# Performance work log

Measured on AMD Instinct MI355X. Metric: run time of the kernel, lower is better.

Reference implementation:

```python
import jax, jax.numpy as jnp
import numpy as np

D_MODEL = 1024
D_INNER = 2048      # expand=2 * d_model
HEADDIM = 64
NHEADS = D_INNER // HEADDIM   # 32 (ssm heads)
D_STATE = 128
D_CONV = 4
CHUNK = 256
D_IN_PROJ = 2 * D_INNER + 2 * D_STATE + NHEADS
CONV_DIM = D_INNER + 2 * D_STATE


def setup_inputs() -> dict:
    key = jax.random.key(0)
    ks = jax.random.split(key, 8)
    sc = lambda f: 1.0 / np.sqrt(f)
    dt_init = jax.random.uniform(ks[3], (NHEADS,), minval=0.001, maxval=0.1)
    return {
        "x": jax.random.normal(ks[0], (2, 4096, D_MODEL), jnp.float32),
        "W_in": jax.random.normal(ks[1], (D_MODEL, D_IN_PROJ), jnp.float32) * sc(D_MODEL),
        "conv_w": jax.random.normal(ks[2], (CONV_DIM, D_CONV), jnp.float32) * sc(D_CONV),
        "conv_b": jnp.zeros((CONV_DIM,), jnp.float32),
        "dt_bias": jnp.log(jnp.expm1(dt_init)),            # inverse softplus
        "A_log": jnp.log(jax.random.uniform(ks[4], (NHEADS,), minval=1.0, maxval=16.0)),
        "D": jnp.ones((NHEADS,), jnp.float32),
        "norm_w": jnp.ones((D_INNER,), jnp.float32),
        "W_out": jax.random.normal(ks[5], (D_INNER, D_MODEL), jnp.float32) * sc(D_INNER),
    }


def _segsum(a):
    # a: (..., T) -> (..., T, T) lower-triangular segment sums, -inf above diag
    T = a.shape[-1]
    cs = jnp.cumsum(a, axis=-1)
    diff = cs[..., :, None] - cs[..., None, :]
    mask = jnp.tril(jnp.ones((T, T), bool))
    return jnp.where(mask, diff, -jnp.inf)


def _ssd(x, A, B, C):
    # x: (b,L,h,p) already scaled by dt; A: (b,L,h) = dt*A_head; B,C: (b,L,n)
    b, L, h, p = x.shape
    nc = L // CHUNK
    xc = x.reshape(b, nc, CHUNK, h, p)
    Ac = A.reshape(b, nc, CHUNK, h).transpose(0, 3, 1, 2)      # (b,h,nc,cl)
    Bc = B.reshape(b, nc, CHUNK, -1)
    Cc = C.reshape(b, nc, CHUNK, -1)
    Acs = jnp.cumsum(Ac, axis=-1)
    # intra-chunk (diagonal) term
    Ldec = jnp.exp(_segsum(Ac))                                # (b,h,nc,cl,cl)
    Yd = jnp.einsum('bcln,bcsn,bhcls,bcshp->bclhp', Cc, Bc, Ldec, xc)
    # chunk end states
    decay_states = jnp.exp(Acs[..., -1:] - Acs)                # (b,h,nc,cl)
    states = jnp.einsum('bcln,bhcl,bclhp->bchpn', Bc, decay_states, xc)
    # inter-chunk recurrence (zero initial state)
    states = jnp.concatenate([jnp.zeros_like(states[:, :1]), states], axis=1)
    A_chunk = jnp.pad(Acs[..., -1], ((0, 0), (0, 0), (1, 0)))  # (b,h,nc+1)
    decay_chunk = jnp.exp(_segsum(A_chunk))                    # (b,h,nc+1,nc+1)
    states = jnp.einsum('bhzc,bchpn->bzhpn', decay_chunk, states)[:, :-1]
    # state -> output term
    out_decay = jnp.exp(Acs)                                   # (b,h,nc,cl)
    Yo = jnp.einsum('bcln,bchpn,bhcl->bclhp', Cc, states, out_decay)
    return (Yd + Yo).reshape(b, L, h, p)


def reference(x, W_in, conv_w, conv_b, dt_bias, A_log, D, norm_w, W_out):
    b, L, _ = x.shape
    zxbcdt = x @ W_in                                          # (b,L,4384)
    z, xBC, dt = jnp.split(zxbcdt, [D_INNER, 2 * D_INNER + 2 * D_STATE], axis=-1)
    # causal depthwise conv1d + silu
    xp = jnp.pad(xBC, ((0, 0), (D_CONV - 1, 0), (0, 0)))
    conv = sum(xp[:, k:k + L] * conv_w[:, k] for k in range(D_CONV)) + conv_b
    xBC = jax.nn.silu(conv)
    xs, B, C = jnp.split(xBC, [D_INNER, D_INNER + D_STATE], axis=-1)
    dt = jax.nn.softplus(dt + dt_bias)                         # (b,L,h)
    A = -jnp.exp(A_log)                                        # (h,)
    xh = xs.reshape(b, L, NHEADS, HEADDIM)
    y = _ssd(xh * dt[..., None], dt * A, B, C)                 # (b,L,h,p)
    y = y + xh * D[None, None, :, None]                        # D skip per head
    y = y.reshape(b, L, D_INNER)
    # gated RMSNorm
    u = y * jax.nn.silu(z)
    u = u * jax.lax.rsqrt(jnp.mean(u * u, axis=-1, keepdims=True) + 1e-5) * norm_w
    return u @ W_out
```

## Files before the change

kernel.cpp:

```cpp
#include <hip/hip_runtime.h>
#include <math.h>

#define B_ 2
#define L_ 4096
#define DM 1024
#define DI 2048
#define HD 64
#define NH 32
#define DS 128
#define CH 256
#define NC 16
#define DPROJ 4384
#define CONVD 2304
#define NGEMM 4352

typedef unsigned short u16;
typedef unsigned int u32;
typedef __attribute__((ext_vector_type(8))) short bf16x8;
typedef __attribute__((ext_vector_type(4))) float f32x4;

__device__ __forceinline__ float silu_(float x) { return x / (1.0f + __expf(-x)); }
__device__ __forceinline__ float us2f(u16 u) {
  union { u32 i; float f; } c; c.i = ((u32)u) << 16; return c.f;
}
__device__ __forceinline__ u16 f2us(float f) {
  union { float f; u32 i; } c; c.f = f;
  u32 i = c.i;
  return (u16)((i + 0x7FFFu + ((i >> 16) & 1u)) >> 16);
}
__device__ __forceinline__ void unpack8(uint4 v, float* o) {
  o[0] = us2f(v.x & 0xffffu); o[1] = us2f(v.x >> 16);
  o[2] = us2f(v.y & 0xffffu); o[3] = us2f(v.y >> 16);
  o[4] = us2f(v.z & 0xffffu); o[5] = us2f(v.z >> 16);
  o[6] = us2f(v.w & 0xffffu); o[7] = us2f(v.w >> 16);
}
__device__ __forceinline__ bf16x8 scale8(bf16x8 a, float s) {
  bf16x8 r;
#pragma unroll
  for (int j = 0; j < 8; ++j) r[j] = (short)f2us(us2f((u16)a[j]) * s);
  return r;
}
__device__ __forceinline__ void gload16(const u16* g, u16* l) {
  __builtin_amdgcn_global_load_lds(
      (const __attribute__((address_space(1))) void*)g,
      (__attribute__((address_space(3))) void*)l, 16, 0, 0);
}

__global__ __launch_bounds__(256) void cvt_t_k(const float* __restrict__ W,
                                               u16* __restrict__ Wt,
                                               int ldW, int ldT) {
  __shared__ float tile[64][65];
  const int t = threadIdx.x;
  const int n0 = blockIdx.x * 64, k0 = blockIdx.y * 64;
#pragma unroll
  for (int i = 0; i < 16; ++i) {
    int j = i * 256 + t;
    int kk = j >> 6, nn = j & 63;
    tile[kk][nn] = W[(size_t)(k0 + kk) * ldW + n0 + nn];
  }
  __syncthreads();
#pragma unroll
  for (int i = 0; i < 16; ++i) {
    int j = i * 256 + t;
    int nn = j >> 6, kk = j & 63;
    Wt[(size_t)(n0 + nn) * ldT + k0 + kk] = f2us(tile[kk][nn]);
  }
}

template <int KDIM, int NTN, int EPI>
__global__ __launch_bounds__(256) void gemm_bf16_k(const u16* __restrict__ A,
                                                   const u16* __restrict__ Bt,
                                                   u16* __restrict__ zb,
                                                   u16* __restrict__ xraw,
                                                   float* __restrict__ outf,
                                                   int nwg) {
  __shared__ u16 pool[(EPI == 1) ? 17408 : 16384];
  u16* Al = pool;
  u16* Bl = pool + 8192;
  const int t = threadIdx.x;
  const int wv = t >> 6, lane = t & 63;
  const int fr = lane & 15, oct = lane >> 4;
  const int wr = wv >> 1, wc = wv & 1;
  const int q = nwg >> 3;
  const int wg = (blockIdx.x & 7) * q + (blockIdx.x >> 3);
  const int bm = wg / NTN, bn = wg % NTN;
  const int m0 = bm * 128, n0 = bn * 128;

  const int lr = lane >> 3, ls = lane & 7;
  const int gslot = (ls ^ lr) * 8;

  f32x4 acc[4][4];
#pragma unroll
  for (int mm = 0; mm < 4; ++mm)
#pragma unroll
    for (int nn = 0; nn < 4; ++nn) acc[mm][nn] = (f32x4){0.f, 0.f, 0.f, 0.f};

  for (int k0 = 0; k0 < KDIM; k0 += 64) {
    if (k0) __syncthreads();
#pragma unroll
    for (int i = 0; i < 4; ++i) {
      const int rowA = wv * 32 + i * 8;
      gload16(&A[(size_t)(m0 + rowA + lr) * KDIM + k0 + gslot], &Al[rowA * 64]);
      gload16(&Bt[(size_t)(n0 + rowA + lr) * KDIM + k0 + gslot], &Bl[rowA * 64]);
    }
    __syncthreads();
#pragma unroll
    for (int kk = 0; kk < 2; ++kk) {
      bf16x8 af[4], bfr[4];
#pragma unroll
      for (int mm = 0; mm < 4; ++mm)
        af[mm] = *(const bf16x8*)&Al[(wr * 64 + mm * 16 + fr) * 64 +
                                     (((kk * 4 + oct) ^ (fr & 7)) * 8)];
#pragma unroll
      for (int nn = 0; nn < 4; ++nn)
        bfr[nn] = *(const bf16x8*)&Bl[(wc * 64 + nn * 16 + fr) * 64 +
                                      (((kk * 4 + oct) ^ (fr & 7)) * 8)];
#pragma unroll
      for (int mm = 0; mm < 4; ++mm)
#pragma unroll
        for (int nn = 0; nn < 4; ++nn)
          acc[mm][nn] = __builtin_amdgcn_mfma_f32_16x16x32_bf16(af[mm], bfr[nn],
                                                                acc[mm][nn], 0, 0, 0);
    }
  }

  if (EPI == 0) {
    const bool isz = (n0 < DI);
#pragma unroll
    for (int P = 0; P < 2; ++P) {
      __syncthreads();
      u16* Oh = pool;
      if (wr == P) {
#pragma unroll
        for (int mm = 0; mm < 4; ++mm)
#pragma unroll
          for (int i = 0; i < 4; ++i) {
            int rloc = mm * 16 + oct * 4 + i;
#pragma unroll
            for (int nn = 0; nn < 4; ++nn)
              Oh[rloc * 136 + wc * 64 + nn * 16 + fr] = f2us(acc[mm][nn][i]);
          }
      }
      __syncthreads();
#pragma unroll
      for (int p = 0; p < 4; ++p) {
        int e = p * 256 + t;
        int row = e >> 4, cs = (e & 15) * 8;
        uint4 v = *(const uint4*)&Oh[row * 136 + cs];
        size_t grow = m0 + P * 64 + row;
        int col = n0 + cs;
        if (isz) *(uint4*)&zb[grow * DI + col] = v;
        else     *(uint4*)&xraw[grow * CONVD + (col - DI)] = v;
      }
    }
  } else {
#pragma unroll
    for (int P = 0; P < 2; ++P) {
      __syncthreads();
      float* Of = (float*)pool;
      if (wr == P) {
#pragma unroll
        for (int mm = 0; mm < 4; ++mm)
#pragma unroll
          for (int i = 0; i < 4; ++i) {
            int rloc = mm * 16 + oct * 4 + i;
#pragma unroll
            for (int nn = 0; nn < 4; ++nn)
              Of[rloc * 132 + wc * 64 + nn * 16 + fr] = acc[mm][nn][i];
          }
      }
      __syncthreads();
#pragma unroll
      for (int p = 0; p < 8; ++p) {
        int e = p * 256 + t;
        int row = e >> 5, c4 = (e & 31) * 4;
        float4 v = *(const float4*)&Of[row * 132 + c4];
        *(float4*)&outf[(size_t)(m0 + P * 64 + row) * DM + n0 + c4] = v;
      }
    }
  }
}

__global__ __launch_bounds__(256) void dt_gemm_k(const float* __restrict__ x,
                                                 const float* __restrict__ W,
                                                 const float* __restrict__ dtb,
                                                 float* __restrict__ dtp,
                                                 u16* __restrict__ xb16) {
  __shared__ float xs[8 * 1024];
  const int t = threadIdx.x;
  const int row0 = blockIdx.x * 8;
#pragma unroll
  for (int i = 0; i < 8; ++i) {
    int j4 = i * 256 + t;
    float4 v = *(const float4*)&x[(size_t)row0 * DM + j4 * 4];
    *(float4*)&xs[j4 * 4] = v;
    u32 lo = (u32)f2us(v.x) | ((u32)f2us(v.y) << 16);
    u32 hi = (u32)f2us(v.z) | ((u32)f2us(v.w) << 16);
    *(uint2*)&xb16[(size_t)row0 * DM + j4 * 4] = make_uint2(lo, hi);
  }
  __syncthreads();
  const int r = t >> 5, h = t & 31;
  float a0 = 0.f, a1 = 0.f, a2 = 0.f, a3 = 0.f;
  const float* wcol = W + (DI + CONVD) + h;
  const float* xr = &xs[r * 1024];
  for (int k = 0; k < 1024; k += 4) {
    float4 xv = *(const float4*)&xr[k];
    a0 += xv.x * wcol[(size_t)(k + 0) * DPROJ];
    a1 += xv.y * wcol[(size_t)(k + 1) * DPROJ];
    a2 += xv.z * wcol[(size_t)(k + 2) * DPROJ];
    a3 += xv.w * wcol[(size_t)(k + 3) * DPROJ];
  }
  float v = (a0 + a1) + (a2 + a3) + dtb[h];
  dtp[(size_t)(row0 + r) * NH + h] = (v > 20.0f) ? v : log1pf(__expf(v));
}

__global__ __launch_bounds__(256) void conv_silu_k(const u16* __restrict__ xraw,
                                                   const float* __restrict__ cw,
                                                   const float* __restrict__ cb,
                                                   u16* __restrict__ xbc) {
  int idx = blockIdx.x * 256 + threadIdx.x;
  int ch8 = idx % (CONVD / 8);
  int bl = idx / (CONVD / 8);
  int l = bl & (L_ - 1);
  int ch = ch8 * 8;
  const u16* src = xraw + (size_t)bl * CONVD + ch;
  float a[8], o[8];
#pragma unroll
  for (int qq = 0; qq < 8; ++qq) a[qq] = cb[ch + qq];
  float w0[8], w1[8], w2[8], w3[8];
#pragma unroll
  for (int qq = 0; qq < 8; ++qq) {
    float4 w = *(const float4*)&cw[(ch + qq) * 4];
    w0[qq] = w.x; w1[qq] = w.y; w2[qq] = w.z; w3[qq] = w.w;
  }
  if (l >= 3) {
    uint4 v = *(const uint4*)&src[-3 * CONVD]; unpack8(v, o);
#pragma unroll
    for (int qq = 0; qq < 8; ++qq) a[qq] += o[qq] * w0[qq];
  }
  if (l >= 2) {
    uint4 v = *(const uint4*)&src[-2 * CONVD]; unpack8(v, o);
#pragma unroll
    for (int qq = 0; qq < 8; ++qq) a[qq] += o[qq] * w1[qq];
  }
  if (l >= 1) {
    uint4 v = *(const uint4*)&src[-CONVD]; unpack8(v, o);
#pragma unroll
    for (int qq = 0; qq < 8; ++qq) a[qq] += o[qq] * w2[qq];
  }
  {
    uint4 v = *(const uint4*)&src[0]; unpack8(v, o);
#pragma unroll
    for (int qq = 0; qq < 8; ++qq) a[qq] += o[qq] * w3[qq];
  }
  uint4 ov;
  ov.x = (u32)f2us(silu_(a[0])) | ((u32)f2us(silu_(a[1])) << 16);
  ov.y = (u32)f2us(silu_(a[2])) | ((u32)f2us(silu_(a[3])) << 16);
  ov.z = (u32)f2us(silu_(a[4])) | ((u32)f2us(silu_(a[5])) << 16);
  ov.w = (u32)f2us(silu_(a[6])) | ((u32)f2us(silu_(a[7])) << 16);
  *(uint4*)&xbc[(size_t)bl * CONVD + ch] = ov;
}

__global__ __launch_bounds__(256) void acs_k(const float* __restrict__ dtp,
                                             const float* __restrict__ A_log,
                                             float* __restrict__ Acs) {
  const int t = threadIdx.x;
  const int lane = t & 63, wv = t >> 6;
  const int idx = blockIdx.x * 4 + wv;
  const int h = (idx >> 4) & (NH - 1);
  const int c = idx & (NC - 1);
  const int b = idx >> 9;
  const float Ah = -__expf(A_log[h]);
  const size_t base = ((size_t)b * L_ + c * CH + lane * 4) * NH + h;
  float v0 = dtp[base] * Ah;
  float v1 = dtp[base + NH] * Ah;
  float v2 = dtp[base + 2 * NH] * Ah;
  float v3 = dtp[base + 3 * NH] * Ah;
  float c1 = v0 + v1, c2 = c1 + v2, c3 = c2 + v3;
  float tot = c3;
#pragma unroll
  for (int off = 1; off < 64; off <<= 1) {
    float p = __shfl_up(tot, off, 64);
    if (lane >= off) tot += p;
  }
  float excl = tot - c3;
  float4 ov = make_float4(excl + v0, excl + c1, excl + c2, excl + c3);
  *(float4*)&Acs[(size_t)idx * CH + lane * 4] = ov;
}

#define SLP 72
__global__ __launch_bounds__(256) void states_k(const u16* __restrict__ xbc,
                                                const float* __restrict__ dtp,
                                                const float* __restrict__ Acs,
                                                u16* __restrict__ st16) {
  __shared__ u16 BtT[128 * SLP];
  __shared__ u16 XtT[64 * SLP];
  const int t = threadIdx.x;
  const int wv = t >> 6, lane = t & 63;
  const int fr = lane & 15, oct = lane >> 4;
  const int h = blockIdx.x & 31, c = (blockIdx.x >> 5) & 15, b = blockIdx.x >> 9;
  const size_t acsb = (((size_t)b * NH + h) * NC + c) * CH;
  const float acs_last = Acs[acsb + (CH - 1)];
  const size_t rowbase = (size_t)b * L_ + c * CH;

  f32x4 acc[2][4];
#pragma unroll
  for (int mt = 0; mt < 2; ++mt)
#pragma unroll
    for (int pt = 0; pt < 4; ++pt) acc[mt][pt] = (f32x4){0.f, 0.f, 0.f, 0.f};

  for (int lt = 0; lt < 4; ++lt) {
    __syncthreads();
#pragma unroll
    for (int i = 0; i < 4; ++i) {
      int ci = i * 256 + t;
      int l = ci >> 4, nk = ci & 15;
      uint4 v = *(const uint4*)&xbc[(rowbase + lt * 64 + l) * CONVD + DI + nk * 8];
      u16 p8[8];
      p8[0] = (u16)(v.x & 0xffffu); p8[1] = (u16)(v.x >> 16);
      p8[2] = (u16)(v.y & 0xffffu); p8[3] = (u16)(v.y >> 16);
      p8[4] = (u16)(v.z & 0xffffu); p8[5] = (u16)(v.z >> 16);
      p8[6] = (u16)(v.w & 0xffffu); p8[7] = (u16)(v.w >> 16);
#pragma unroll
      for (int qq = 0; qq < 8; ++qq) {
        int r = nk * 8 + qq;
        BtT[r * SLP + ((((l >> 3) ^ (r >> 3)) & 7) << 3) + (l & 7)] = p8[qq];
      }
    }
#pragma unroll
    for (int i = 0; i < 2; ++i) {
      int ci = i * 256 + t;
      int l = ci >> 3, pk = ci & 7;
      size_t row = rowbase + lt * 64 + l;
      uint4 v = *(const uint4*)&xbc[row * CONVD + h * HD + pk * 8];
      float d = dtp[row * NH + h] * __expf(acs_last - Acs[acsb + lt * 64 + l]);
      float o[8]; unpack8(v, o);
#pragma unroll
      for (int qq = 0; qq < 8; ++qq) {
        int r = pk * 8 + qq;
        XtT[r * SLP + ((((l >> 3) ^ (r >> 3)) & 7) << 3) + (l & 7)] = f2us(o[qq] * d);
      }
    }
    __syncthreads();
#pragma unroll
    for (int ks = 0; ks < 2; ++ks) {
      bf16x8 afr[2], bfr[4];
#pragma unroll
      for (int mt = 0; mt < 2; ++mt) {
        int r = wv * 32 + mt * 16 + fr;
        afr[mt] = *(const bf16x8*)&BtT[r * SLP + ((((ks * 4 + oct) ^ (r >> 3)) & 7) << 3)];
      }
#pragma unroll
      for (int pt = 0; pt < 4; ++pt) {
        int r = pt * 16 + fr;
        bfr[pt] = *(const bf16x8*)&XtT[r * SLP + ((((ks * 4 + oct) ^ (r >> 3)) & 7) << 3)];
      }
#pragma unroll
      for (int mt = 0; mt < 2; ++mt)
#pragma unroll
        for (int pt = 0; pt < 4; ++pt)
          acc[mt][pt] = __builtin_amdgcn_mfma_f32_16x16x32_bf16(afr[mt], bfr[pt],
                                                                acc[mt][pt], 0, 0, 0);
    }
  }
  size_t sbase = (((size_t)b * NC + c) * NH + h) * (size_t)(HD * DS);
#pragma unroll
  for (int mt = 0; mt < 2; ++mt)
#pragma unroll
    for (int pt = 0; pt < 4; ++pt) {
      int p = pt * 16 + fr;
      int n0 = wv * 32 + mt * 16 + oct * 4;
      u32 lo = (u32)f2us(acc[mt][pt][0]) | ((u32)f2us(acc[mt][pt][1]) << 16);
      u32 hi = (u32)f2us(acc[mt][pt][2]) | ((u32)f2us(acc[mt][pt][3]) << 16);
      *(uint2*)&st16[sbase + (size_t)p * DS + n0] = make_uint2(lo, hi);
    }
}

__global__ __launch_bounds__(256) void scan_k(u16* __restrict__ st16,
                                              const float* __restrict__ Acs) {
  const int t = threadIdx.x;
  const int seg = blockIdx.x & 15;
  const int bh = blockIdx.x >> 4;
  const int h = bh & 31, b = bh >> 5;
  const int e2 = seg * 256 + t;
  const size_t acssb = ((size_t)b * NH + h) * NC * CH;
  float run0 = 0.0f, run1 = 0.0f;
#pragma unroll
  for (int c = 0; c < NC; ++c) {
    float dAl = __expf(Acs[acssb + (size_t)c * CH + (CH - 1)]);
    size_t e = (((size_t)b * NC + c) * NH + h) * (size_t)(HD * DS) + e2 * 2;
    u32 v = *(const u32*)&st16[e];
    float s0 = us2f((u16)(v & 0xffffu)), s1 = us2f((u16)(v >> 16));
    *(u32*)&st16[e] = (u32)f2us(run0) | ((u32)f2us(run1) << 16);
    run0 = fmaf(dAl, run0, s0);
    run1 = fmaf(dAl, run1, s1);
  }
}

#define SP 72
#define XOFF 8192
#define POFF 12800
__global__ __launch_bounds__(512, 4) void ssd_out_k(const u16* __restrict__ xbc,
                                                    const float* __restrict__ dtp,
                                                    const float* __restrict__ Acs,
                                                    const u16* __restrict__ st16,
                                                    const float* __restrict__ Dvec,
                                                    u16* __restrict__ y) {
  __shared__ u16 pool[31232];
  __shared__ float acs_s[256];
  const int t = threadIdx.x;
  const int w = t >> 6, lane = t & 63;
  const int fr = lane & 15, oct = lane >> 4;
  const int h = blockIdx.x & 31, c = (blockIdx.x >> 5) & 15, b = blockIdx.x >> 9;
  const size_t acsb = (((size_t)b * NH + h) * NC + c) * CH;
  const size_t rowbase = (size_t)b * L_ + c * CH;
  if (t < 256) acs_s[t] = Acs[acsb + t];
  const size_t sb = (((size_t)b * NC + c) * NH + h) * (size_t)(HD * DS);
#pragma unroll
  for (int i = 0; i < 2; ++i) {
    int ci = i * 512 + t; int p = ci >> 4, nk = ci & 15;
    uint4 v = *(const uint4*)&st16[sb + (size_t)p * DS + nk * 8];
    *(uint4*)&pool[p * 136 + nk * 8] = v;
  }
  __syncthreads();
  bf16x8 ca[2][4];
#pragma unroll
  for (int mt = 0; mt < 2; ++mt)
#pragma unroll
    for (int kk = 0; kk < 4; ++kk)
      ca[mt][kk] = *(const bf16x8*)&xbc[(rowbase + w * 32 + mt * 16 + fr) * CONVD +
                                        DI + DS + kk * 32 + oct * 8];
  f32x4 acc_y[2][4];
#pragma unroll
  for (int mt = 0; mt < 2; ++mt)
#pragma unroll
    for (int pp4 = 0; pp4 < 4; ++pp4) acc_y[mt][pp4] = (f32x4){0.f, 0.f, 0.f, 0.f};

  {
    float eL0 = __expf(acs_s[w * 32 + fr]);
    float eL1 = __expf(acs_s[w * 32 + 16 + fr]);
#pragma unroll
    for (int kk = 0; kk < 4; ++kk) {
      bf16x8 c0 = scale8(ca[0][kk], eL0);
      bf16x8 c1 = scale8(ca[1][kk], eL1);
#pragma unroll
      for (int pp4 = 0; pp4 < 4; ++pp4) {
        bf16x8 sf = *(const bf16x8*)&pool[(pp4 * 16 + fr) * 136 + kk * 32 + oct * 8];
        acc_y[0][pp4] = __builtin_amdgcn_mfma_f32_16x16x32_bf16(c0, sf, acc_y[0][pp4], 0, 0, 0);
        acc_y[1][pp4] = __builtin_amdgcn_mfma_f32_16x16x32_bf16(c1, sf, acc_y[1][pp4], 0, 0, 0);
      }
    }
  }

  const int stmax = w >> 1, delta = (w & 1) << 5;
  for (int st = 0; st < 4; ++st) {
    __syncthreads();
#pragma unroll
    for (int i = 0; i < 2; ++i) {
      int ci = i * 512 + t; int ll = ci >> 4, ck = ci & 15;
      uint4 v = *(const uint4*)&xbc[(rowbase + st * 64 + ll) * CONVD + DI + ck * 8];
      *(uint4*)&pool[ll * 128 + ((ck * 8) ^ ((ll & 7) << 3))] = v;
    }
    {
      int s = t >> 3, pk = t & 7;
      size_t row = rowbase + st * 64 + s;
      uint4 v = *(const uint4*)&xbc[row * CONVD + h * HD + pk * 8];
      float d = dtp[row * NH + h];
      float o[8]; unpack8(v, o);
#pragma unroll
      for (int qq = 0; qq < 8; ++qq) {
        int r = pk * 8 + qq;
        pool[XOFF + r * SP + ((((s >> 3) ^ (r >> 3)) & 7) << 3) + (s & 7)] = f2us(o[qq] * d);
      }
    }
    __syncthreads();
    if (st > stmax) continue;
    const bool diag = (st == stmax);
#pragma unroll
    for (int ss4 = 0; ss4 < 4; ++ss4) {
      bf16x8 bbf[4];
#pragma unroll
      for (int kk = 0; kk < 4; ++kk)
        bbf[kk] = *(const bf16x8*)&pool[(ss4 * 16 + fr) * 128 +
                                        ((kk * 32 + oct * 8) ^ ((fr & 7) << 3))];
      int s_in = ss4 * 16 + fr;
      float aS = acs_s[st * 64 + s_in];
#pragma unroll
      for (int mt = 0; mt < 2; ++mt) {
        f32x4 sacc = (f32x4){0.f, 0.f, 0.f, 0.f};
#pragma unroll
        for (int kk = 0; kk < 4; ++kk)
          sacc = __builtin_amdgcn_mfma_f32_16x16x32_bf16(ca[mt][kk], bbf[kk], sacc, 0, 0, 0);
#pragma unroll
        for (int i = 0; i < 4; ++i) {
          int r = mt * 16 + oct * 4 + i;
          float aL = acs_s[w * 32 + r];
          float wgt = (!diag || (s_in <= r + delta)) ? __expf(aL - aS) : 0.0f;
          pool[POFF + w * 2304 + r * SP + s_in] = f2us(sacc[i] * wgt);
        }
      }
    }
    bf16x8 pa[2][2];
#pragma unroll
    for (int mt = 0; mt < 2; ++mt)
#pragma unroll
      for (int k2 = 0; k2 < 2; ++k2)
        pa[mt][k2] = *(const bf16x8*)&pool[POFF + w * 2304 + (mt * 16 + fr) * SP +
                                           k2 * 32 + oct * 8];
#pragma unroll
    for (int pp4 = 0; pp4 < 4; ++pp4) {
      int rx = pp4 * 16 + fr, xg = rx >> 3;
      bf16x8 xb0 = *(const bf16x8*)&pool[XOFF + rx * SP + (((oct) ^ xg) & 7) * 8];
      bf16x8 xb1 = *(const bf16x8*)&pool[XOFF + rx * SP + (((4 + oct) ^ xg) & 7) * 8];
#pragma unroll
      for (int mt = 0; mt < 2; ++mt) {
        acc_y[mt][pp4] = __builtin_amdgcn_mfma_f32_16x16x32_bf16(pa[mt][0], xb0, acc_y[mt][pp4], 0, 0, 0);
        acc_y[mt][pp4] = __builtin_amdgcn_mfma_f32_16x16x32_bf16(pa[mt][1], xb1, acc_y[mt][pp4], 0, 0, 0);
      }
    }
  }

  const float Dh = Dvec[h];
#pragma unroll
  for (int mt = 0; mt < 2; ++mt)
#pragma unroll
    for (int i = 0; i < 4; ++i) {
      size_t row = rowbase + w * 32 + mt * 16 + oct * 4 + i;
#pragma unroll
      for (int pp4 = 0; pp4 < 4; ++pp4) {
        int col = h * HD + pp4 * 16 + fr;
        float xs = us2f(xbc[row * CONVD + col]);
        y[row * DI + col] = f2us(acc_y[mt][pp4][i] + Dh * xs);
      }
    }
}

__global__ __launch_bounds__(256) void gnorm_k(const u16* __restrict__ zb,
                                               const float* __restrict__ nw,
                                               u16* __restrict__ y) {
  const int row = blockIdx.x, t = threadIdx.x;
  const u16* zr = zb + (size_t)row * DI;
  u16* yr = y + (size_t)row * DI;
  uint4 zv = *(const uint4*)&zr[t * 8];
  uint4 yv = *(const uint4*)&yr[t * 8];
  float uz[8], uy[8];
  unpack8(zv, uz); unpack8(yv, uy);
  float u[8], ssum = 0.0f;
#pragma unroll
  for (int j = 0; j < 8; ++j) { u[j] = uy[j] * silu_(uz[j]); ssum += u[j] * u[j]; }
#pragma unroll
  for (int off = 32; off >= 1; off >>= 1) ssum += __shfl_xor(ssum, off, 64);
  __shared__ float red[4];
  if ((t & 63) == 0) red[t >> 6] = ssum;
  __syncthreads();
  float sc = rsqrtf((red[0] + red[1] + red[2] + red[3]) * (1.0f / DI) + 1e-5f);
  float4 w0 = *(const float4*)&nw[t * 8];
  float4 w1 = *(const float4*)&nw[t * 8 + 4];
  float o0 = u[0] * sc * w0.x, o1 = u[1] * sc * w0.y, o2 = u[2] * sc * w0.z, o3 = u[3] * sc * w0.w;
  float o4 = u[4] * sc * w1.x, o5 = u[5] * sc * w1.y, o6 = u[6] * sc * w1.z, o7 = u[7] * sc * w1.w;
  uint4 ov;
  ov.x = (u32)f2us(o0) | ((u32)f2us(o1) << 16);
  ov.y = (u32)f2us(o2) | ((u32)f2us(o3) << 16);
  ov.z = (u32)f2us(o4) | ((u32)f2us(o5) << 16);
  ov.w = (u32)f2us(o6) | ((u32)f2us(o7) << 16);
  *(uint4*)&yr[t * 8] = ov;
}

extern "C" void kernel_launch(void* const* d_in, const int* in_sizes, int n_in,
                              void* d_out, int out_size, void* d_ws, size_t ws_size,
                              hipStream_t stream) {
  const float* x      = (const float*)d_in[0];
  const float* W_in   = (const float*)d_in[1];
  const float* conv_w = (const float*)d_in[2];
  const float* conv_b = (const float*)d_in[3];
  const float* dt_b   = (const float*)d_in[4];
  const float* A_log  = (const float*)d_in[5];
  const float* Dvec   = (const float*)d_in[6];
  const float* norm_w = (const float*)d_in[7];
  const float* W_out  = (const float*)d_in[8];
  float* out = (float*)d_out;

  u16* zb       = (u16*)d_ws;
  u16* xbc      = zb + (size_t)B_ * L_ * DI;
  float* dtp    = (float*)(xbc + (size_t)B_ * L_ * CONVD);
  float* Acs    = dtp + (size_t)B_ * L_ * NH;
  u16* stregion = (u16*)(Acs + (size_t)B_ * NH * L_);
  u16* uni      = stregion + (size_t)B_ * NC * NH * HD * DS * 2;
  u16* xraw = uni;
  u16* y    = uni;

  u16* xb16     = stregion;
  u16* wint     = stregion + (size_t)B_ * L_ * DM;
  u16* states16 = stregion;
  u16* woutt    = stregion;

  const int Mrows = B_ * L_;

  dt_gemm_k<<<Mrows / 8, 256, 0, stream>>>(x, W_in, dt_b, dtp, xb16);
  cvt_t_k<<<dim3(NGEMM / 64, DM / 64), 256, 0, stream>>>(W_in, wint, DPROJ, DM);

  const int nwg_in = (Mrows / 128) * (NGEMM / 128);
  gemm_bf16_k<DM, NGEMM / 128, 0><<<nwg_in, 256, 0, stream>>>(
      xb16, wint, zb, xraw, nullptr, nwg_in);

  conv_silu_k<<<(Mrows * (CONVD / 8)) / 256, 256, 0, stream>>>(xraw, conv_w, conv_b, xbc);
  acs_k<<<(B_ * NH * NC) / 4, 256, 0, stream>>>(dtp, A_log, Acs);
  states_k<<<B_ * NC * NH, 256, 0, stream>>>(xbc, dtp, Acs, states16);
  scan_k<<<B_ * NH * 16, 256, 0, stream>>>(states16, Acs);
  ssd_out_k<<<B_ * NC * NH, 512, 0, stream>>>(xbc, dtp, Acs, states16, Dvec, y);
  gnorm_k<<<Mrows, 256, 0, stream>>>(zb, norm_w, y);

  cvt_t_k<<<dim3(DM / 64, DI / 64), 256, 0, stream>>>(W_out, woutt, DM, DI);
  const int nwg_out = (Mrows / 128) * (DM / 128);
  gemm_bf16_k<DI, DM / 128, 1><<<nwg_out, 256, 0, stream>>>(
      y, woutt, nullptr, nullptr, out, nwg_out);
}
```

Before: 361.5 us.

## Add 256x256-tile 8-wave GEMM with double-buffered LDS for input projection

Replaces the 128x128-tile input-projection GEMM with a new kernel using 256x256 output tiles, 512 threads, double-buffered LDS with XOR swizzle, and staged global loads interleaved with MFMA quarters. It also raises wave priority around the MFMA bursts. The larger tile halves global/LDS traffic per FLOP, but the grid shrinks to 32x17=544 workgroups and uses 128KB LDS per block, which limits occupancy and may leave tail imbalance across CUs.

New measurement: 366.3 us. About the same (+1.3%).

```diff
diff --git a/kernel.cpp b/kernel.cpp
--- a/kernel.cpp
+++ b/kernel.cpp
@@ -64,6 +64,127 @@
     int j = i * 256 + t;
     int nn = j >> 6, kk = j & 63;
     Wt[(size_t)(n0 + nn) * ldT + k0 + kk] = f2us(tile[kk][nn]);
+  }
+}
+
+template <int KDIM, int NTN>
+__global__ __launch_bounds__(512, 2) void gemm256_k(const u16* __restrict__ A,
+                                                    const u16* __restrict__ Bt,
+                                                    u16* __restrict__ zb,
+                                                    u16* __restrict__ xraw,
+                                                    int nwg) {
+  __shared__ u16 lds[65536];
+  const int t = threadIdx.x;
+  const int lane = t & 63;
+  const int fr = lane & 15, oct = lane >> 4;
+  const int w = t >> 6;
+  const int wr = w >> 2, wc = w & 3;
+  const int w64base = t & ~63;
+  const int q8 = nwg >> 3;
+  const int wg = (blockIdx.x & 7) * q8 + (blockIdx.x >> 3);
+  const int bm = wg / NTN, bn = wg % NTN;
+  const int m0 = bm * 256, n0 = bn * 256;
+  const int NT = KDIM >> 6;
+
+  f32x4 acc[8][4];
+#pragma unroll
+  for (int i = 0; i < 8; ++i)
+#pragma unroll
+    for (int j = 0; j < 4; ++j) acc[i][j] = (f32x4){0.f, 0.f, 0.f, 0.f};
+
+#define STAGE256(tt, qq)                                                        \
+  {                                                                             \
+    u16* dst = lds + (((tt) & 1) << 15) + (((qq) & 1) << 14) + (((qq) >> 1) << 13); \
+    const u16* src = ((qq) & 1) ? Bt : A;                                       \
+    const int brow = (((qq) & 1) ? n0 : m0) + (((qq) >> 1) << 7);               \
+    const int k0 = (tt) << 6;                                                   \
+    _Pragma("unroll")                                                           \
+    for (int j_ = 0; j_ < 2; ++j_) {                                            \
+      int e_ = j_ * 512 + t;                                                    \
+      int r_ = e_ >> 3, s_ = e_ & 7;                                            \
+      gload16(&src[(size_t)(brow + r_) * KDIM + k0 + ((s_ ^ (r_ & 7)) << 3)],   \
+              &dst[(j_ * 512 + w64base) * 8]);                                  \
+    }                                                                           \
+  }
+
+  STAGE256(0, 0); STAGE256(0, 1); STAGE256(0, 2); STAGE256(0, 3);
+  asm volatile("s_waitcnt vmcnt(4)" ::: "memory");
+  __builtin_amdgcn_s_barrier();
+
+  for (int tt = 0; tt < NT; ++tt) {
+    const u16* Ab = lds + ((tt & 1) << 15);
+    const u16* Bb = Ab + 16384;
+#pragma unroll
+    for (int q = 0; q < 4; ++q) {
+      const int mh = q & 1, nh = q >> 1;
+      bf16x8 af[4][2], bfv[2][2];
+#pragma unroll
+      for (int i = 0; i < 4; ++i) {
+        int r = mh * 128 + wr * 64 + i * 16 + fr;
+#pragma unroll
+        for (int kk = 0; kk < 2; ++kk)
+          af[i][kk] = *(const bf16x8*)&Ab[r * 64 + (((kk * 4 + oct) ^ (fr & 7)) << 3)];
+      }
+#pragma unroll
+      for (int j = 0; j < 2; ++j) {
+        int r = nh * 128 + wc * 32 + j * 16 + fr;
+#pragma unroll
+        for (int kk = 0; kk < 2; ++kk)
+          bfv[j][kk] = *(const bf16x8*)&Bb[r * 64 + (((kk * 4 + oct) ^ (fr & 7)) << 3)];
+      }
+      if (tt + 1 < NT) {
+        STAGE256(tt + 1, q);
+        asm volatile("s_waitcnt vmcnt(4)" ::: "memory");
+      } else {
+        asm volatile("s_waitcnt vmcnt(0)" ::: "memory");
+      }
+      __builtin_amdgcn_s_barrier();
+      __builtin_amdgcn_s_setprio(1);
+#pragma unroll
+      for (int kk = 0; kk < 2; ++kk)
+#pragma unroll
+        for (int i = 0; i < 4; ++i)
+#pragma unroll
+          for (int j = 0; j < 2; ++j)
+            acc[mh * 4 + i][nh * 2 + j] = __builtin_amdgcn_mfma_f32_16x16x32_bf16(
+                af[i][kk], bfv[j][kk], acc[mh * 4 + i][nh * 2 + j], 0, 0, 0);
+      __builtin_amdgcn_s_setprio(0);
+      __builtin_amdgcn_s_barrier();
+    }
+  }
+#undef STAGE256
+
+  const bool isz = (n0 < DI);
+  u16* Oh = lds;
+#pragma unroll
+  for (int P = 0; P < 4; ++P) {
+    __syncthreads();
+    if (wr == (P & 1)) {
+      const int mhP = P >> 1;
+#pragma unroll
+      for (int i = 0; i < 4; ++i) {
+        int mf = mhP * 4 + i;
+        int rbase = i * 16 + oct * 4;
+#pragma unroll
+        for (int ri = 0; ri < 4; ++ri)
+#pragma unroll
+          for (int nf = 0; nf < 4; ++nf) {
+            int cloc = (nf >> 1) * 128 + wc * 32 + (nf & 1) * 16 + fr;
+            Oh[(rbase + ri) * 264 + cloc] = f2us(acc[mf][nf][ri]);
+          }
+      }
+    }
+    __syncthreads();
+#pragma unroll
+    for (int p = 0; p < 4; ++p) {
+      int e = p * 512 + t;
+      int row = e >> 5, cs = (e & 31) * 8;
+      uint4 v = *(const uint4*)&Oh[row * 264 + cs];
+      size_t grow = m0 + P * 64 + row;
+      int col = n0 + cs;
+      if (isz) *(uint4*)&zb[grow * DI + col] = v;
+      else     *(uint4*)&xraw[grow * CONVD + (col - DI)] = v;
+    }
   }
 }
 
@@ -599,9 +720,8 @@
   dt_gemm_k<<<Mrows / 8, 256, 0, stream>>>(x, W_in, dt_b, dtp, xb16);
   cvt_t_k<<<dim3(NGEMM / 64, DM / 64), 256, 0, stream>>>(W_in, wint, DPROJ, DM);
 
-  const int nwg_in = (Mrows / 128) * (NGEMM / 128);
-  gemm_bf16_k<DM, NGEMM / 128, 0><<<nwg_in, 256, 0, stream>>>(
-      xb16, wint, zb, xraw, nullptr, nwg_in);
+  const int nwg_in = (Mrows / 256) * (NGEMM / 256);
+  gemm256_k<DM, NGEMM / 256><<<nwg_in, 512, 0, stream>>>(xb16, wint, zb, xraw, nwg_in);
 
   conv_silu_k<<<(Mrows * (CONVD / 8)) / 256, 256, 0, stream>>>(xraw, conv_w, conv_b, xbc);
   acs_k<<<(B_ * NH * NC) / 4, 256, 0, stream>>>(dtp, A_log, Acs);
```
